# Performance work log

Hardware: AMD Instinct MI355X
Metric: run time of the kernel (lower is better)

The kernel has to match this reference:

```python
import jax, jax.numpy as jnp
import numpy as np


def setup_inputs() -> dict:
    key = jax.random.key(0)
    k1, k2, k3, k4, k5 = jax.random.split(key, 5)
    S, B = 512, 256
    E, H, C = 256, 1024, 10
    x = jax.random.randint(k1, (S, B), 0, 10, dtype=jnp.int32)
    emb = jax.random.normal(k2, (10, E), dtype=jnp.float32)
    # orthogonal-ish init is irrelevant for correctness baseline; use scaled normals
    W_hx = jax.random.normal(k3, (E, H), dtype=jnp.float32) / np.sqrt(E)
    W_hh = jax.random.normal(k4, (H, H), dtype=jnp.float32) / np.sqrt(H)
    W_ph = jax.random.normal(k5, (H, C), dtype=jnp.float32) / np.sqrt(H)
    b_h = jnp.zeros((H,), dtype=jnp.float32)
    b_p = jnp.zeros((C,), dtype=jnp.float32)
    return {"x": x, "emb": emb, "W_hx": W_hx, "W_hh": W_hh,
            "W_ph": W_ph, "b_h": b_h, "b_p": b_p}


def reference(x, emb, W_hx, W_hh, W_ph, b_h, b_p):
    S, B = x.shape
    H = W_hh.shape[0]
    # Precompute input projection for all steps in one big GEMM: [S,B,H]
    x_proj = jnp.einsum('sbe,eh->sbh', emb[x], W_hx) + b_h

    def step(state, xp_t):
        state = jnp.tanh(xp_t + state @ W_hh)
        return state, None

    init = jnp.zeros((B, H), dtype=x_proj.dtype)
    state, _ = jax.lax.scan(step, init, x_proj)
    # original detaches the final state before the output projection
    state = jax.lax.stop_gradient(state)
    out = state @ W_ph + b_p  # [B, C]
    return out
```

## Files before the change

kernel.cpp:

```cpp
#include <hip/hip_runtime.h>
#include <hip/hip_bf16.h>


typedef __attribute__((ext_vector_type(8))) short short8;
typedef __attribute__((ext_vector_type(4))) float f32x4;

#define S_LEN 512
#define HDIM  1024
#define NVOC  10

#define OFF_WF    0u
#define OFF_PROJ  2097152u
#define OFF_STBF  2138112u
#define OFF_STF   3186688u
#define OFF_FLAGS 4235264u
#define OFF_XCD   4251648u
#define OFF_SETUP 4252672u

__global__ void zero_flags_k(unsigned int* flags) {
    int id = blockIdx.x * 256 + threadIdx.x;
    if (id < 4096 + 256 + 16) flags[id] = 0u;
}

__global__ void proj_k(const float* __restrict__ emb, const float* __restrict__ W_hx,
                       const float* __restrict__ b_h, float* __restrict__ proj) {
    int id = blockIdx.x * 256 + threadIdx.x;
    if (id >= NVOC * HDIM) return;
    int v = id >> 10, h = id & 1023;
    float a = b_h[h];
    #pragma unroll 8
    for (int e = 0; e < 256; ++e) a += emb[v * 256 + e] * W_hx[e * HDIM + h];
    proj[id] = a;
}

static __device__ inline unsigned short f2bf(float f) {
    unsigned u = __builtin_bit_cast(unsigned, f);
    return (unsigned short)((u + 0x7fffu + ((u >> 16) & 1u)) >> 16);
}

__global__ void packw_k(const float* __restrict__ W_hh, unsigned short* __restrict__ Wf) {
    int idx = blockIdx.x * 256 + threadIdx.x;
    int lane = idx & 63, kk = (idx >> 6) & 31, nt = idx >> 11;
    int k0 = kk * 32 + (lane >> 4) * 8;
    int col = nt * 16 + (lane & 15);
    short8 v;
    #pragma unroll
    for (int j = 0; j < 8; ++j) v[j] = (short)f2bf(W_hh[(k0 + j) * HDIM + col]);
    *(short8*)(Wf + (size_t)idx * 8) = v;
}

__global__ __launch_bounds__(256, 1) void rnn_steps_k(
    const int* __restrict__ x, const unsigned short* __restrict__ Wf,
    const float* __restrict__ proj, unsigned short* __restrict__ stbf,
    float* __restrict__ stf, unsigned int* __restrict__ flags,
    unsigned int* __restrict__ xcdmap, unsigned int* __restrict__ setupf)
{
    const int bid = blockIdx.x;
    const int g   = ((bid & 7) << 1) | ((bid >> 3) & 1);
    const int wgn = bid >> 4;
    const int tid = threadIdx.x;
    const int wave = tid >> 6, lane = tid & 63;
    const int b0 = g << 4;
    const int nt = (wgn << 2) + wave;
    const int n0 = nt << 4;
    const int wg_n0 = wgn << 6;
    const int row = lane & 15;
    const int kl  = lane >> 4;

    __shared__ __align__(16) char Abuf[32768];
    __shared__ unsigned char xl[S_LEN * 16];
    __shared__ float pl[NVOC * 64];
    __shared__ unsigned uni_sh;

    unsigned xcd;
    asm("s_getreg_b32 %0, hwreg(HW_REG_XCC_ID)" : "=s"(xcd));
    if (tid == 0) {
        xcdmap[(g << 4) + wgn] = xcd;
        __hip_atomic_fetch_add(setupf + g, 1u, __ATOMIC_RELEASE, __HIP_MEMORY_SCOPE_AGENT);
        while (__hip_atomic_load(setupf + g, __ATOMIC_ACQUIRE, __HIP_MEMORY_SCOPE_AGENT) < 16u) {}
        unsigned u = 1u;
        for (int i = 0; i < 16; ++i) {
            unsigned v = __hip_atomic_load(xcdmap + (g << 4) + i,
                                           __ATOMIC_RELAXED, __HIP_MEMORY_SCOPE_AGENT);
            u &= (unsigned)(v == xcd);
        }
        uni_sh = u;
    }

    for (int i = tid; i < S_LEN * 16; i += 256)
        xl[i] = (unsigned char)x[((i >> 4) << 8) + b0 + (i & 15)];
    for (int i = tid; i < NVOC * 64; i += 256)
        pl[i] = proj[(i >> 6) * HDIM + wg_n0 + (i & 63)];

    short8 bfr[32];
    const short8* wp = (const short8*)Wf;
    #pragma unroll
    for (int kk = 0; kk < 32; ++kk)
        bfr[kk] = wp[((nt << 5) + kk) * 64 + lane];

    __syncthreads();
    const bool uniform = (uni_sh != 0u);

    const int sw = (row & 7) << 4;
    const int abase = row << 11;
    const int klb = kl << 4;
    unsigned int* myslot = flags + (g << 8) + (wgn << 4);

    for (int s = 0; s < S_LEN; ++s) {
        f32x4 acc0 = {0.f, 0.f, 0.f, 0.f};
        f32x4 acc1 = acc0, acc2 = acc0, acc3 = acc0;
        if (s > 0) {
            if (tid < 16) {
                const unsigned int* fp = flags + (g << 8) + (tid << 4);
                while (__hip_atomic_load(fp, __ATOMIC_RELAXED, __HIP_MEMORY_SCOPE_AGENT)
                       < (unsigned)s) {}
            }
            __syncthreads();
            const char* src = (const char*)stbf + (((s - 1) & 1) << 19) + (g << 15);
            if (uniform) {
                #pragma unroll
                for (int it = 0; it < 8; ++it) {
                    int o = (it * 256 + tid) * 16;
                    int arow = o >> 11;
                    int soff = (arow << 11) + ((o & 2047) ^ ((arow & 7) << 4));
                    __builtin_amdgcn_global_load_lds(
                        (const __attribute__((address_space(1))) void*)(src + soff),
                        (__attribute__((address_space(3))) void*)(Abuf + it * 4096 + wave * 1024),
                        16, 0, 1);
                }
            } else {
                #pragma unroll
                for (int it = 0; it < 8; ++it) {
                    int o = (it * 256 + tid) * 16;
                    int arow = o >> 11;
                    int soff = (arow << 11) + ((o & 2047) ^ ((arow & 7) << 4));
                    __builtin_amdgcn_global_load_lds(
                        (const __attribute__((address_space(1))) void*)(src + soff),
                        (__attribute__((address_space(3))) void*)(Abuf + it * 4096 + wave * 1024),
                        16, 0, 17);
                }
            }
            __syncthreads();
            #pragma unroll
            for (int kk = 0; kk < 32; kk += 4) {
                short8 a0 = *(const short8*)(Abuf + abase + ((((kk + 0) << 6) + klb) ^ sw));
                short8 a1 = *(const short8*)(Abuf + abase + ((((kk + 1) << 6) + klb) ^ sw));
                short8 a2 = *(const short8*)(Abuf + abase + ((((kk + 2) << 6) + klb) ^ sw));
                short8 a3 = *(const short8*)(Abuf + abase + ((((kk + 3) << 6) + klb) ^ sw));
                acc0 = __builtin_amdgcn_mfma_f32_16x16x32_bf16(a0, bfr[kk + 0], acc0, 0, 0, 0);
                acc1 = __builtin_amdgcn_mfma_f32_16x16x32_bf16(a1, bfr[kk + 1], acc1, 0, 0, 0);
                acc2 = __builtin_amdgcn_mfma_f32_16x16x32_bf16(a2, bfr[kk + 2], acc2, 0, 0, 0);
                acc3 = __builtin_amdgcn_mfma_f32_16x16x32_bf16(a3, bfr[kk + 3], acc3, 0, 0, 0);
            }
        }
        f32x4 accs = acc0 + acc1 + acc2 + acc3;
        #pragma unroll
        for (int j = 0; j < 4; ++j) {
            int r = (kl << 2) + j;
            int xv = xl[(s << 4) + r];
            float p = pl[(xv << 6) + (wave << 4) + row];
            float z = accs[j] + p;
            z = fminf(15.f, fmaxf(-15.f, z));
            float e = exp2f(z * 2.885390082f);
            float th = (e - 1.f) / (e + 1.f);
            if (s < S_LEN - 1) {
                stbf[((s & 1) << 18) + ((b0 + r) << 10) + n0 + row] = f2bf(th);
            } else {
                stf[((b0 + r) << 10) + n0 + row] = th;
            }
        }
        if (s < S_LEN - 1) {
            __syncthreads();
            if (tid == 0) {
                if (uniform) {
                    __hip_atomic_store(myslot, (unsigned)(s + 1),
                                       __ATOMIC_RELAXED, __HIP_MEMORY_SCOPE_AGENT);
                } else {
                    __hip_atomic_store(myslot, (unsigned)(s + 1),
                                       __ATOMIC_RELEASE, __HIP_MEMORY_SCOPE_AGENT);
                }
            }
        }
    }
}

__global__ void outproj_k(const float* __restrict__ stf, const float* __restrict__ W_ph,
                          const float* __restrict__ b_p, float* __restrict__ out) {
    int b = blockIdx.x, t = threadIdx.x;
    float acc[10];
    #pragma unroll
    for (int c = 0; c < 10; ++c) acc[c] = 0.f;
    for (int h = t; h < HDIM; h += 256) {
        float sv = stf[b * HDIM + h];
        const float* w = W_ph + h * 10;
        #pragma unroll
        for (int c = 0; c < 10; ++c) acc[c] += sv * w[c];
    }
    __shared__ float red[256][10];
    #pragma unroll
    for (int c = 0; c < 10; ++c) red[t][c] = acc[c];
    __syncthreads();
    for (int off = 128; off > 0; off >>= 1) {
        if (t < off) {
            #pragma unroll
            for (int c = 0; c < 10; ++c) red[t][c] += red[t + off][c];
        }
        __syncthreads();
    }
    if (t < 10) out[b * 10 + t] = red[0][t] + b_p[t];
}

extern "C" void kernel_launch(void* const* d_in, const int* in_sizes, int n_in,
                              void* d_out, int out_size, void* d_ws, size_t ws_size,
                              hipStream_t stream) {
    const int*   x    = (const int*)d_in[0];
    const float* emb  = (const float*)d_in[1];
    const float* W_hx = (const float*)d_in[2];
    const float* W_hh = (const float*)d_in[3];
    const float* W_ph = (const float*)d_in[4];
    const float* b_h  = (const float*)d_in[5];
    const float* b_p  = (const float*)d_in[6];

    char* ws = (char*)d_ws;
    unsigned short* Wf     = (unsigned short*)(ws + OFF_WF);
    float*          proj   = (float*)(ws + OFF_PROJ);
    unsigned short* stbf   = (unsigned short*)(ws + OFF_STBF);
    float*          stf    = (float*)(ws + OFF_STF);
    unsigned int*   flags  = (unsigned int*)(ws + OFF_FLAGS);
    unsigned int*   xcdmap = (unsigned int*)(ws + OFF_XCD);
    unsigned int*   setupf = (unsigned int*)(ws + OFF_SETUP);

    zero_flags_k<<<18, 256, 0, stream>>>(flags);
    proj_k<<<40, 256, 0, stream>>>(emb, W_hx, b_h, proj);
    packw_k<<<512, 256, 0, stream>>>(W_hh, Wf);
    rnn_steps_k<<<256, 256, 0, stream>>>(x, Wf, proj, stbf, stf, flags, xcdmap, setupf);
    outproj_k<<<256, 256, 0, stream>>>(stf, W_ph, b_p, (float*)d_out);
}
```

Baseline: 1.339 ms.

## Overlap per-producer flag polling with chunked state loads into double-buffered LDS

The step loop used to wait for all 16 producer workgroups' flags before issuing one bulk copy of the previous state into LDS. Now each wave polls four specific producer flags and, as soon as each one is ready, loads that producer's 64-column chunk into LDS. This lets data movement start while other producers are still finishing. The LDS A buffer is double-buffered by step parity and re-laid out per producer chunk with a new XOR swizzle, and the MFMA loop reads match the new layout. The projection table row stride is padded to 68 to avoid bank conflicts. In exchange, every wave now spins on global flags, and the added LDS usage and changed indexing add risk.

```diff
diff --git a/kernel.cpp b/kernel.cpp
--- a/kernel.cpp
+++ b/kernel.cpp
@@ -67,9 +67,9 @@
     const int row = lane & 15;
     const int kl  = lane >> 4;
 
-    __shared__ __align__(16) char Abuf[32768];
+    __shared__ __align__(16) char Abuf[2][32768];
     __shared__ unsigned char xl[S_LEN * 16];
-    __shared__ float pl[NVOC * 64];
+    __shared__ float pl[NVOC * 68];
     __shared__ unsigned uni_sh;
 
     unsigned xcd;
@@ -89,8 +89,11 @@
 
     for (int i = tid; i < S_LEN * 16; i += 256)
         xl[i] = (unsigned char)x[((i >> 4) << 8) + b0 + (i & 15)];
-    for (int i = tid; i < NVOC * 64; i += 256)
-        pl[i] = proj[(i >> 6) * HDIM + wg_n0 + (i & 63)];
+    if (tid < 64) {
+        #pragma unroll
+        for (int v = 0; v < NVOC; ++v)
+            pl[v * 68 + tid] = proj[v * HDIM + wg_n0 + tid];
+    }
 
     short8 bfr[32];
     const short8* wp = (const short8*)Wf;
@@ -101,56 +104,60 @@
     __syncthreads();
     const bool uniform = (uni_sh != 0u);
 
-    const int sw = (row & 7) << 4;
-    const int abase = row << 11;
-    const int klb = kl << 4;
+    const int srow = lane >> 3;
+    const int scol = ((lane & 7) ^ srow) << 4;
+    const int abase2 = row << 7;
+    const int axor   = (row & 7) << 4;
+    const int aklb   = kl << 4;
     unsigned int* myslot = flags + (g << 8) + (wgn << 4);
 
     for (int s = 0; s < S_LEN; ++s) {
         f32x4 acc0 = {0.f, 0.f, 0.f, 0.f};
         f32x4 acc1 = acc0, acc2 = acc0, acc3 = acc0;
         if (s > 0) {
-            if (tid < 16) {
-                const unsigned int* fp = flags + (g << 8) + (tid << 4);
-                while (__hip_atomic_load(fp, __ATOMIC_RELAXED, __HIP_MEMORY_SCOPE_AGENT)
-                       < (unsigned)s) {}
-            }
-            __syncthreads();
-            const char* src = (const char*)stbf + (((s - 1) & 1) << 19) + (g << 15);
-            if (uniform) {
-                #pragma unroll
-                for (int it = 0; it < 8; ++it) {
-                    int o = (it * 256 + tid) * 16;
-                    int arow = o >> 11;
-                    int soff = (arow << 11) + ((o & 2047) ^ ((arow & 7) << 4));
-                    __builtin_amdgcn_global_load_lds(
-                        (const __attribute__((address_space(1))) void*)(src + soff),
-                        (__attribute__((address_space(3))) void*)(Abuf + it * 4096 + wave * 1024),
+            char* dst = Abuf[s & 1];
+            const char* srcbase = (const char*)stbf + (((s - 1) & 1) << 19) + (g << 15);
+            #pragma unroll
+            for (int i = 0; i < 4; ++i) {
+                const int p = (wave << 2) + i;
+                const unsigned int* fp = flags + (g << 8) + (p << 4);
+                unsigned fv;
+                do {
+                    fv = __hip_atomic_load(fp, __ATOMIC_RELAXED, __HIP_MEMORY_SCOPE_AGENT);
+                } while (fv < (unsigned)s);
+                const char* csrc = srcbase + (p << 7) + scol + srow * 2048;
+                if (uniform) {
+                    __builtin_amdgcn_global_load_lds(
+                        (const __attribute__((address_space(1))) void*)(csrc),
+                        (__attribute__((address_space(3))) void*)(dst + (p << 11)),
                         16, 0, 1);
-                }
-            } else {
-                #pragma unroll
-                for (int it = 0; it < 8; ++it) {
-                    int o = (it * 256 + tid) * 16;
-                    int arow = o >> 11;
-                    int soff = (arow << 11) + ((o & 2047) ^ ((arow & 7) << 4));
-                    __builtin_amdgcn_global_load_lds(
-                        (const __attribute__((address_space(1))) void*)(src + soff),
-                        (__attribute__((address_space(3))) void*)(Abuf + it * 4096 + wave * 1024),
+                    __builtin_amdgcn_global_load_lds(
+                        (const __attribute__((address_space(1))) void*)(csrc + 8 * 2048),
+                        (__attribute__((address_space(3))) void*)(dst + (p << 11) + 1024),
+                        16, 0, 1);
+                } else {
+                    __builtin_amdgcn_global_load_lds(
+                        (const __attribute__((address_space(1))) void*)(csrc),
+                        (__attribute__((address_space(3))) void*)(dst + (p << 11)),
+                        16, 0, 17);
+                    __builtin_amdgcn_global_load_lds(
+                        (const __attribute__((address_space(1))) void*)(csrc + 8 * 2048),
+                        (__attribute__((address_space(3))) void*)(dst + (p << 11) + 1024),
                         16, 0, 17);
                 }
             }
             __syncthreads();
+            const char* ab = dst + abase2;
             #pragma unroll
-            for (int kk = 0; kk < 32; kk += 4) {
-                short8 a0 = *(const short8*)(Abuf + abase + ((((kk + 0) << 6) + klb) ^ sw));
-                short8 a1 = *(const short8*)(Abuf + abase + ((((kk + 1) << 6) + klb) ^ sw));
-                short8 a2 = *(const short8*)(Abuf + abase + ((((kk + 2) << 6) + klb) ^ sw));
-                short8 a3 = *(const short8*)(Abuf + abase + ((((kk + 3) << 6) + klb) ^ sw));
-                acc0 = __builtin_amdgcn_mfma_f32_16x16x32_bf16(a0, bfr[kk + 0], acc0, 0, 0, 0);
-                acc1 = __builtin_amdgcn_mfma_f32_16x16x32_bf16(a1, bfr[kk + 1], acc1, 0, 0, 0);
-                acc2 = __builtin_amdgcn_mfma_f32_16x16x32_bf16(a2, bfr[kk + 2], acc2, 0, 0, 0);
-                acc3 = __builtin_amdgcn_mfma_f32_16x16x32_bf16(a3, bfr[kk + 3], acc3, 0, 0, 0);
+            for (int p = 0; p < 16; p += 2) {
+                short8 a0 = *(const short8*)(ab + ((p + 0) << 11) + ((aklb) ^ axor));
+                short8 a1 = *(const short8*)(ab + ((p + 0) << 11) + ((64 + aklb) ^ axor));
+                short8 a2 = *(const short8*)(ab + ((p + 1) << 11) + ((aklb) ^ axor));
+                short8 a3 = *(const short8*)(ab + ((p + 1) << 11) + ((64 + aklb) ^ axor));
+                acc0 = __builtin_amdgcn_mfma_f32_16x16x32_bf16(a0, bfr[2 * p + 0], acc0, 0, 0, 0);
+                acc1 = __builtin_amdgcn_mfma_f32_16x16x32_bf16(a1, bfr[2 * p + 1], acc1, 0, 0, 0);
+                acc2 = __builtin_amdgcn_mfma_f32_16x16x32_bf16(a2, bfr[2 * p + 2], acc2, 0, 0, 0);
+                acc3 = __builtin_amdgcn_mfma_f32_16x16x32_bf16(a3, bfr[2 * p + 3], acc3, 0, 0, 0);
             }
         }
         f32x4 accs = acc0 + acc1 + acc2 + acc3;
@@ -158,7 +165,7 @@
         for (int j = 0; j < 4; ++j) {
             int r = (kl << 2) + j;
             int xv = xl[(s << 4) + r];
-            float p = pl[(xv << 6) + (wave << 4) + row];
+            float p = pl[xv * 68 + (wave << 4) + row];
             float z = accs[j] + p;
             z = fminf(15.f, fmaxf(-15.f, z));
             float e = exp2f(z * 2.885390082f);
```

After: 1.324 ms. No clear change (-1.1%).
